# Kernel optimization log

Hardware: AMD Instinct MI355X
Metric: run time of the kernel (lower is better)

Reference implementation:

```python
import jax, jax.numpy as jnp
import numpy as np

B, S, D, H, E = 4, 2048, 512, 8, 4  # batch, seq, embed, heads, expand
HD = D // H


def setup_inputs() -> dict:
    key = jax.random.key(0)
    ks = jax.random.split(key, 9)
    s = lambda k, shape, fan: jax.random.normal(k, shape, jnp.float32) * (fan ** -0.5)
    return {
        "x": jax.random.normal(ks[0], (B, S, D), jnp.float32),
        "Wq": s(ks[1], (D, D), D),
        "Wk": s(ks[2], (D, D), D),
        "Wv": s(ks[3], (D, D), D),
        "Wo": s(ks[4], (D, D), D),
        "W1": s(ks[5], (D, D * E), D),
        "b1": jnp.zeros((D * E,), jnp.float32),
        "W2": s(ks[6], (D * E, D), D * E),
        "b2": jnp.zeros((D,), jnp.float32),
    }


def _encoder_layer(x, Wq, Wk, Wv, Wo, W1, b1, W2, b2):
    # NOTE: source computes InstanceNorm1d twice but discards both results -> no-ops.
    scale = D ** -0.25  # applied to BOTH q and k (net 1/sqrt(embed_dim))
    q = (x @ Wq).reshape(B, S, H, HD).transpose(0, 2, 1, 3) * scale  # [B,H,S,hd]
    k = (x @ Wk).reshape(B, S, H, HD).transpose(0, 2, 1, 3) * scale
    v = (x @ Wv).reshape(B, S, H, HD).transpose(0, 2, 1, 3)
    scores = jnp.einsum('bhqd,bhkd->bhqk', q, k)  # [B,H,S,S]
    attn = jax.nn.softmax(scores, axis=-1)
    o = jnp.einsum('bhqk,bhkd->bhqd', attn, v)  # [B,H,S,hd]
    o = o.transpose(0, 2, 1, 3).reshape(B, S, D)
    x = o @ Wo + x  # residual 1
    h = jax.nn.gelu(x @ W1 + b1, approximate=True)  # torch GELU(approximate='tanh')
    return h @ W2 + b2 + x  # residual 2 (dropout=0, eval)


def reference(x, Wq, Wk, Wv, Wo, W1, b1, W2, b2):
    return _encoder_layer(x, Wq, Wk, Wv, Wo, W1, b1, W2, b2)
```

## Files before the change

kernel.cpp:

```cpp
#include <hip/hip_runtime.h>
#include <hip/hip_bf16.h>


typedef __bf16 bf16;
typedef __attribute__((ext_vector_type(8))) __bf16 bf16x8;
typedef __attribute__((ext_vector_type(4))) __bf16 bf16x4;
typedef __attribute__((ext_vector_type(4))) float f32x4;
typedef __attribute__((ext_vector_type(16))) float f32x16;
typedef __attribute__((ext_vector_type(2))) unsigned int u32x2;
typedef __attribute__((ext_vector_type(4))) unsigned int u32x4;

#define LOG2E 1.4426950408889634f
#define SCORE_SCALE 0.044194173824159216f
#define SCALE_L2E (SCORE_SCALE * LOG2E)
#define FIXED_M 12.0f

#if __has_builtin(__builtin_amdgcn_exp2f)
#define EXP2(x) __builtin_amdgcn_exp2f(x)
#else
#define EXP2(x) exp2f(x)
#endif

__device__ __forceinline__ void gl_lds16(const bf16* g, bf16* l) {
  __builtin_amdgcn_global_load_lds(
      (const __attribute__((address_space(1))) unsigned int*)g,
      (__attribute__((address_space(3))) unsigned int*)l, 16, 0, 0);
}

template <int N>
__device__ __forceinline__ void wait_vm_barrier() {
  if constexpr (N == 0)
    asm volatile("s_waitcnt vmcnt(0)\ns_barrier" ::: "memory");
  else if constexpr (N == 3)
    asm volatile("s_waitcnt vmcnt(3)\ns_barrier" ::: "memory");
  else if constexpr (N == 4)
    asm volatile("s_waitcnt vmcnt(4)\ns_barrier" ::: "memory");
}

__device__ __forceinline__ float gelu_tanh(float x) {
  float u = 0.7978845608028654f * (x + 0.044715f * x * x * x);
  float e = EXP2(u * (2.0f * LOG2E));
  float th = 1.0f - 2.0f / (e + 1.0f);
  return 0.5f * x * (1.0f + th);
}

__device__ __forceinline__ f32x4 mfma_bf16(bf16x8 a, bf16x8 b, f32x4 c) {
  return __builtin_amdgcn_mfma_f32_16x16x32_bf16(a, b, c, 0, 0, 0);
}
__device__ __forceinline__ f32x16 mfma32x16(bf16x8 a, bf16x8 b, f32x16 c) {
  return __builtin_amdgcn_mfma_f32_32x32x16_bf16(a, b, c, 0, 0, 0);
}

__device__ __forceinline__ void plswap(unsigned int& a, unsigned int& b) {
  asm volatile("v_permlane32_swap_b32 %0, %1" : "+v"(a), "+v"(b));
}

template <int MODE, typename OutT, int TN>
__global__ __launch_bounds__(256, 2) void gemm_bt(
    const bf16* __restrict__ A, const bf16* __restrict__ Bt,
    OutT* __restrict__ C, const float* __restrict__ bias,
    const float* __restrict__ resf, const bf16* __restrict__ resb,
    bf16* __restrict__ vt, int M, int N, int K) {
  constexpr int MI = (TN == 128) ? 4 : 2;
  constexpr int NBUF = (TN == 128) ? 2 : 3;
  __shared__ __align__(16) bf16 sA[NBUF][128 * 32];
  __shared__ __align__(16) bf16 sB[NBUF][TN * 32];
  const int tid = threadIdx.x;
  const int lane = tid & 63;
  const int quad = lane >> 4, lc = lane & 15;
  const int wave = tid >> 6;
  const int wr = (TN == 128) ? (wave >> 1) : wave;
  const int wc = (TN == 128) ? (wave & 1) : 0;
  const int m0 = blockIdx.y * 128, n0 = blockIdx.x * TN;

  const int srow = tid >> 2;
  const int kc = (tid & 3) * 8;
  const bf16* Ag1 = A + (size_t)(m0 + srow) * K + kc;
  const bf16* Ag2 = A + (size_t)(m0 + 64 + srow) * K + kc;
  const bf16* Bg1 = Bt + (size_t)(n0 + srow) * K + kc;
  const bf16* Bg2 = Bt + (size_t)(n0 + 64 + srow) * K + kc;
  const int o1 = tid * 8, o2 = (tid + 256) * 8;

  f32x4 acc[MI][4];
#pragma unroll
  for (int mi = 0; mi < MI; ++mi)
#pragma unroll
    for (int ni = 0; ni < 4; ++ni) acc[mi][ni] = (f32x4){0.f, 0.f, 0.f, 0.f};

  const int kIters = K >> 5;

  if constexpr (TN == 128) {
    gl_lds16(Ag1, sA[0] + o1);
    gl_lds16(Ag2, sA[0] + o2);
    gl_lds16(Bg1, sB[0] + o1);
    gl_lds16(Bg2, sB[0] + o2);
    Ag1 += 32; Ag2 += 32; Bg1 += 32; Bg2 += 32;

    for (int kt = 0; kt < kIters; ++kt) {
      __syncthreads();
      const bf16* cA = sA[kt & 1];
      const bf16* cB = sB[kt & 1];
      if (kt + 1 < kIters) {
        bf16* nA = sA[(kt + 1) & 1];
        bf16* nB = sB[(kt + 1) & 1];
        gl_lds16(Ag1, nA + o1);
        gl_lds16(Ag2, nA + o2);
        gl_lds16(Bg1, nB + o1);
        gl_lds16(Bg2, nB + o2);
        Ag1 += 32; Ag2 += 32; Bg1 += 32; Bg2 += 32;
      }
      bf16x8 af[MI], bfm[4];
#pragma unroll
      for (int i = 0; i < MI; ++i)
        af[i] = *(const bf16x8*)(cA +
                                 ((wr * 64 + i * 16 + lc) * 32 + quad * 8));
#pragma unroll
      for (int i = 0; i < 4; ++i)
        bfm[i] =
            *(const bf16x8*)(cB + ((wc * 64 + i * 16 + lc) * 32 + quad * 8));
#pragma unroll
      for (int mi = 0; mi < MI; ++mi)
#pragma unroll
        for (int ni = 0; ni < 4; ++ni)
          acc[mi][ni] = mfma_bf16(af[mi], bfm[ni], acc[mi][ni]);
    }
  } else {
    auto stage = [&](int t) {
      bf16* a = sA[t % 3];
      bf16* bb = sB[t % 3];
      gl_lds16(Ag1 + t * 32, a + o1);
      gl_lds16(Ag2 + t * 32, a + o2);
      gl_lds16(Bg1 + t * 32, bb + o1);
    };
    stage(0);
    stage(1);
    for (int kt = 0; kt < kIters; ++kt) {
      if (kt + 1 < kIters)
        wait_vm_barrier<3>();
      else
        wait_vm_barrier<0>();
      if (kt + 2 < kIters) stage(kt + 2);
      const bf16* cA = sA[kt % 3];
      const bf16* cB = sB[kt % 3];
      bf16x8 af[MI], bfm[4];
#pragma unroll
      for (int i = 0; i < MI; ++i)
        af[i] = *(const bf16x8*)(cA +
                                 ((wr * 32 + i * 16 + lc) * 32 + quad * 8));
#pragma unroll
      for (int i = 0; i < 4; ++i)
        bfm[i] = *(const bf16x8*)(cB + ((i * 16 + lc) * 32 + quad * 8));
#pragma unroll
      for (int mi = 0; mi < MI; ++mi)
#pragma unroll
        for (int ni = 0; ni < 4; ++ni)
          acc[mi][ni] = mfma_bf16(af[mi], bfm[ni], acc[mi][ni]);
    }
  }

  if constexpr (MODE == 0) {
    if (n0 >= 1024) {
#pragma unroll
      for (int mi = 0; mi < MI; ++mi) {
        const int row0 = m0 + wr * (16 * MI) + mi * 16 + quad * 4;
        const int bb = row0 >> 11, s0 = row0 & 2047;
#pragma unroll
        for (int ni = 0; ni < 4; ++ni) {
          const int col = n0 + wc * 64 + ni * 16 + lc;
          const int hh = (col >> 6) & 7, d = col & 63;
          bf16x4 pb;
#pragma unroll
          for (int r = 0; r < 4; ++r) pb[r] = (bf16)acc[mi][ni][r];
          *(bf16x4*)(vt + ((size_t)((bb * 8 + hh) * 64 + d)) * 2048 + s0) = pb;
        }
      }
      return;
    }
  }
#pragma unroll
  for (int mi = 0; mi < MI; ++mi) {
#pragma unroll
    for (int r = 0; r < 4; ++r) {
      const int row = m0 + wr * (16 * MI) + mi * 16 + quad * 4 + r;
#pragma unroll
      for (int ni = 0; ni < 4; ++ni) {
        const int col = n0 + wc * 64 + ni * 16 + lc;
        const size_t idx = (size_t)row * N + col;
        float v = acc[mi][ni][r];
        if (MODE == 1) v += resf[idx];
        if (MODE == 2) v = gelu_tanh(v + bias[col]);
        if (MODE == 3) v += bias[col] + (float)resb[idx];
        C[idx] = (OutT)v;
      }
    }
  }
}

__global__ __launch_bounds__(256, 2) void flash_attn(
    const bf16* __restrict__ QKV, const bf16* __restrict__ Vt,
    bf16* __restrict__ O) {
  const int tid = threadIdx.x;
  const int lane = tid & 63, wave = tid >> 6;
  const int lo5 = lane & 31, hi = lane >> 5;
  const int lin = blockIdx.y * 16 + blockIdx.x;
  const int xcd = lin & 7, slot = lin >> 3;
  const int bh = xcd * 4 + (slot >> 4);
  const int qt = slot & 15;
  const int b = bh >> 3, h = bh & 7;
  const int q0 = qt * 128 + wave * 32;

  __shared__ __align__(16) bf16 sK[3][4096];
  __shared__ __align__(16) bf16 sV[3][4096];

  const bf16* Qrow = QKV + (size_t)(b * 2048 + q0 + lo5) * 1536 + h * 64;
  bf16x8 qf[4];
#pragma unroll
  for (int i = 0; i < 4; ++i) qf[i] = *(const bf16x8*)(Qrow + i * 16 + hi * 8);

  const int colsw = (((lane & 7) ^ (lane >> 3)) << 3);
  const bf16* Kg0 = QKV + (size_t)b * 2048 * 1536 + 512 + (size_t)h * 64 +
                    (size_t)(wave * 16 + (lane >> 3)) * 1536 + colsw;
  const bf16* Vg0 = Vt + (size_t)bh * 64 * 2048 +
                    (size_t)(wave * 16 + (lane >> 3)) * 2048 + colsw;
  const int stag = wave * 1024;
  const int m7 = lo5 & 7;

  f32x16 oacc[2];
  oacc[0] = (f32x16)(0.f);
  oacc[1] = (f32x16)(0.f);
  float rs0 = 0.f, rs1 = 0.f, rs2 = 0.f, rs3 = 0.f;

  auto stage = [&](int t) {
    bf16* dk = sK[t % 3] + stag;
    bf16* dv = sV[t % 3] + stag;
    gl_lds16(Kg0 + (size_t)t * 64 * 1536, dk);
    gl_lds16(Kg0 + (size_t)(t * 64 + 8) * 1536, dk + 512);
    gl_lds16(Vg0 + t * 64, dv);
    gl_lds16(Vg0 + t * 64 + 8 * 2048, dv + 512);
  };
  stage(0);
  stage(1);

  for (int kt = 0; kt < 32; ++kt) {
    if (kt == 31)
      wait_vm_barrier<0>();
    else
      wait_vm_barrier<4>();
    if (kt + 2 < 32) stage(kt + 2);
    const bf16* cK = sK[kt % 3];
    const bf16* cV = sV[kt % 3];

    bf16x8 vf[2][4];
#pragma unroll
    for (int dh = 0; dh < 2; ++dh) {
      const int Rd = dh * 32 + lo5;
#pragma unroll
      for (int w = 0; w < 4; ++w)
        vf[dh][w] =
            *(const bf16x8*)(cV + Rd * 64 + (((2 * w + hi) ^ m7) << 3));
    }

    bf16x8 paw[4];
#pragma unroll
    for (int hl = 0; hl < 2; ++hl) {
      f32x16 st = (f32x16)(0.f);
      const int R = hl * 32 + lo5;
      __builtin_amdgcn_s_setprio(1);
#pragma unroll
      for (int i = 0; i < 4; ++i) {
        bf16x8 kf =
            *(const bf16x8*)(cK + R * 64 + (((2 * i + hi) ^ m7) << 3));
        st = mfma32x16(kf, qf[i], st);
      }
      __builtin_amdgcn_s_setprio(0);
      unsigned int q32[4][2];
#pragma unroll
      for (int g = 0; g < 4; ++g) {
        bf16x4 pb;
        float p0 = EXP2(st[4 * g + 0] * SCALE_L2E - FIXED_M);
        float p1 = EXP2(st[4 * g + 1] * SCALE_L2E - FIXED_M);
        float p2 = EXP2(st[4 * g + 2] * SCALE_L2E - FIXED_M);
        float p3 = EXP2(st[4 * g + 3] * SCALE_L2E - FIXED_M);
        rs0 += p0; rs1 += p1; rs2 += p2; rs3 += p3;
        pb[0] = (bf16)p0; pb[1] = (bf16)p1; pb[2] = (bf16)p2; pb[3] = (bf16)p3;
        u32x2 w2 = __builtin_bit_cast(u32x2, pb);
        q32[g][0] = w2[0];
        q32[g][1] = w2[1];
      }
#pragma unroll
      for (int t = 0; t < 2; ++t) {
        unsigned int a0 = q32[2 * t][0], a1 = q32[2 * t][1];
        unsigned int b0 = q32[2 * t + 1][0], b1 = q32[2 * t + 1][1];
        plswap(a0, b0);
        plswap(a1, b1);
        u32x4 f = {a0, a1, b0, b1};
        paw[hl * 2 + t] = __builtin_bit_cast(bf16x8, f);
      }
    }

    __builtin_amdgcn_s_setprio(1);
#pragma unroll
    for (int dh = 0; dh < 2; ++dh)
#pragma unroll
      for (int w = 0; w < 4; ++w)
        oacc[dh] = mfma32x16(paw[w], vf[dh][w], oacc[dh]);
    __builtin_amdgcn_s_setprio(0);
  }

  float rsum = (rs0 + rs1) + (rs2 + rs3);
  rsum += __shfl_xor(rsum, 32, 64);
  const size_t obase = (size_t)(b * 2048 + q0) * 512 + h * 64;
#pragma unroll
  for (int r = 0; r < 16; ++r) {
    const int qloc = (r & 3) + 8 * (r >> 2) + 4 * hi;
    const float inv = 1.0f / __shfl(rsum, qloc, 64);
#pragma unroll
    for (int dh = 0; dh < 2; ++dh)
      O[obase + (size_t)qloc * 512 + dh * 32 + lo5] =
          (bf16)(oacc[dh][r] * inv);
  }
}

__global__ __launch_bounds__(256) void prep(
    const float* __restrict__ x, const float* __restrict__ Wq,
    const float* __restrict__ Wk, const float* __restrict__ Wv,
    const float* __restrict__ Wo, const float* __restrict__ W1,
    const float* __restrict__ W2, bf16* __restrict__ xb,
    bf16* __restrict__ WqkvT, bf16* __restrict__ WoT, bf16* __restrict__ W1T,
    bf16* __restrict__ W2T) {
  const int bid = blockIdx.x;
  if (bid < 4096) {
    const size_t i = ((size_t)bid * 256 + threadIdx.x) * 4;
    const float4 v = *(const float4*)(x + i);
    bf16x4 o;
    o[0] = (bf16)v.x; o[1] = (bf16)v.y; o[2] = (bf16)v.z; o[3] = (bf16)v.w;
    *(bf16x4*)(xb + i) = o;
    return;
  }
  const int t = bid - 4096;
  const float* in;
  bf16* out;
  int in_ld, out_ld, bx, by;
  if (t < 1024) {
    const int q = t >> 8, r = t & 255;
    bx = r & 15; by = r >> 4; in_ld = 512; out_ld = 512;
    in = (q == 0) ? Wq : (q == 1) ? Wk : (q == 2) ? Wv : Wo;
    out = (q == 0) ? WqkvT
          : (q == 1) ? WqkvT + 512 * 512
          : (q == 2) ? WqkvT + 2 * 512 * 512
                     : WoT;
  } else if (t < 2048) {
    const int r = t - 1024;
    bx = r & 63; by = r >> 6; in_ld = 2048; out_ld = 512;
    in = W1; out = W1T;
  } else {
    const int r = t - 2048;
    bx = r & 15; by = r >> 4; in_ld = 512; out_ld = 2048;
    in = W2; out = W2T;
  }
  __shared__ __align__(16) bf16 tl[32][33];
  const int tx = threadIdx.x & 31, ty = threadIdx.x >> 5;
  const int n0 = bx * 32, k0 = by * 32;
#pragma unroll
  for (int i = 0; i < 4; ++i)
    tl[ty + 8 * i][tx] = (bf16)in[(size_t)(k0 + ty + 8 * i) * in_ld + n0 + tx];
  __syncthreads();
#pragma unroll
  for (int i = 0; i < 4; ++i)
    out[(size_t)(n0 + ty + 8 * i) * out_ld + k0 + tx] = tl[tx][ty + 8 * i];
}

extern "C" void kernel_launch(void* const* d_in, const int* in_sizes, int n_in,
                              void* d_out, int out_size, void* d_ws,
                              size_t ws_size, hipStream_t stream) {
  const float* x = (const float*)d_in[0];
  const float* Wq = (const float*)d_in[1];
  const float* Wk = (const float*)d_in[2];
  const float* Wv = (const float*)d_in[3];
  const float* Wo = (const float*)d_in[4];
  const float* W1 = (const float*)d_in[5];
  const float* b1 = (const float*)d_in[6];
  const float* W2 = (const float*)d_in[7];
  const float* b2 = (const float*)d_in[8];
  float* out = (float*)d_out;

  char* ws = (char*)d_ws;
  size_t off = 0;
  auto alloc = [&](size_t bytes) {
    char* p = ws + off;
    off += (bytes + 255) & ~(size_t)255;
    return p;
  };
  bf16* WqkvT = (bf16*)alloc(1536ULL * 512 * 2);
  bf16* WoT = (bf16*)alloc(512ULL * 512 * 2);
  bf16* W1T = (bf16*)alloc(2048ULL * 512 * 2);
  bf16* W2T = (bf16*)alloc(512ULL * 2048 * 2);
  bf16* xb = (bf16*)alloc(8192ULL * 512 * 2);
  bf16* QKV = (bf16*)alloc(8192ULL * 1536 * 2);
  bf16* Vt = (bf16*)alloc(32ULL * 64 * 2048 * 2);
  bf16* attn = (bf16*)alloc(8192ULL * 512 * 2);
  bf16* x2 = xb;
  bf16* hbuf = QKV;

  const dim3 tb(256);
  prep<<<dim3(7168), tb, 0, stream>>>(x, Wq, Wk, Wv, Wo, W1, W2, xb, WqkvT,
                                      WoT, W1T, W2T);
  gemm_bt<0, bf16, 128><<<dim3(12, 64), tb, 0, stream>>>(
      xb, WqkvT, QKV, nullptr, nullptr, nullptr, Vt, 8192, 1536, 512);
  flash_attn<<<dim3(16, 32), tb, 0, stream>>>(QKV, Vt, attn);
  gemm_bt<1, bf16, 64><<<dim3(8, 64), tb, 0, stream>>>(
      attn, WoT, x2, nullptr, x, nullptr, nullptr, 8192, 512, 512);
  gemm_bt<2, bf16, 128><<<dim3(16, 64), tb, 0, stream>>>(
      x2, W1T, hbuf, b1, nullptr, nullptr, nullptr, 8192, 2048, 512);
  gemm_bt<3, float, 64><<<dim3(8, 64), tb, 0, stream>>>(
      hbuf, W2T, out, b2, nullptr, x2, nullptr, 8192, 512, 2048);
}
```

Baseline: 247.0 us.

## Load K/V tiles directly into registers instead of staging through LDS

Replaces the triple-buffered LDS staging of K and V tiles with direct global-to-register loads, double-buffered in two register sets (A/B). This removes LDS traffic and the barriers between iterations. It also interleaves the softmax of the second half-tile with the PV MFMAs of the first half. In exchange, each wave fetches K/V separately from global memory or L2 with no sharing across the block's waves, which raises global traffic about fourfold. It also increases register pressure, which may hurt occupancy under launch_bounds(256,2).

Result: slower. 328.0 us (+32.8%).

```diff
diff --git a/kernel.cpp b/kernel.cpp
--- a/kernel.cpp
+++ b/kernel.cpp
@@ -209,102 +209,97 @@
   const int b = bh >> 3, h = bh & 7;
   const int q0 = qt * 128 + wave * 32;
 
-  __shared__ __align__(16) bf16 sK[3][4096];
-  __shared__ __align__(16) bf16 sV[3][4096];
-
   const bf16* Qrow = QKV + (size_t)(b * 2048 + q0 + lo5) * 1536 + h * 64;
   bf16x8 qf[4];
 #pragma unroll
   for (int i = 0; i < 4; ++i) qf[i] = *(const bf16x8*)(Qrow + i * 16 + hi * 8);
 
-  const int colsw = (((lane & 7) ^ (lane >> 3)) << 3);
-  const bf16* Kg0 = QKV + (size_t)b * 2048 * 1536 + 512 + (size_t)h * 64 +
-                    (size_t)(wave * 16 + (lane >> 3)) * 1536 + colsw;
-  const bf16* Vg0 = Vt + (size_t)bh * 64 * 2048 +
-                    (size_t)(wave * 16 + (lane >> 3)) * 2048 + colsw;
-  const int stag = wave * 1024;
-  const int m7 = lo5 & 7;
+  const bf16* Kl = QKV + (size_t)b * 2048 * 1536 + 512 + (size_t)h * 64 +
+                   (size_t)lo5 * 1536 + hi * 8;
+  const bf16* Vl = Vt + (size_t)bh * 64 * 2048 + (size_t)lo5 * 2048 + hi * 8;
 
   f32x16 oacc[2];
   oacc[0] = (f32x16)(0.f);
   oacc[1] = (f32x16)(0.f);
   float rs0 = 0.f, rs1 = 0.f, rs2 = 0.f, rs3 = 0.f;
 
-  auto stage = [&](int t) {
-    bf16* dk = sK[t % 3] + stag;
-    bf16* dv = sV[t % 3] + stag;
-    gl_lds16(Kg0 + (size_t)t * 64 * 1536, dk);
-    gl_lds16(Kg0 + (size_t)(t * 64 + 8) * 1536, dk + 512);
-    gl_lds16(Vg0 + t * 64, dv);
-    gl_lds16(Vg0 + t * 64 + 8 * 2048, dv + 512);
-  };
-  stage(0);
-  stage(1);
-
-  for (int kt = 0; kt < 32; ++kt) {
-    if (kt == 31)
-      wait_vm_barrier<0>();
-    else
-      wait_vm_barrier<4>();
-    if (kt + 2 < 32) stage(kt + 2);
-    const bf16* cK = sK[kt % 3];
-    const bf16* cV = sV[kt % 3];
-
-    bf16x8 vf[2][4];
-#pragma unroll
-    for (int dh = 0; dh < 2; ++dh) {
-      const int Rd = dh * 32 + lo5;
+  bf16x8 kfA[2][4], vfA[2][4], kfB[2][4], vfB[2][4];
+
+  auto loadT = [&](bf16x8(&kf)[2][4], bf16x8(&vf)[2][4], int t) {
+#pragma unroll
+    for (int hl = 0; hl < 2; ++hl)
+#pragma unroll
+      for (int i = 0; i < 4; ++i)
+        kf[hl][i] = *(const bf16x8*)(Kl + ((size_t)(t * 64 + hl * 32)) * 1536 +
+                                     i * 16);
+#pragma unroll
+    for (int dh = 0; dh < 2; ++dh)
 #pragma unroll
       for (int w = 0; w < 4; ++w)
         vf[dh][w] =
-            *(const bf16x8*)(cV + Rd * 64 + (((2 * w + hi) ^ m7) << 3));
-    }
-
-    bf16x8 paw[4];
-#pragma unroll
-    for (int hl = 0; hl < 2; ++hl) {
-      f32x16 st = (f32x16)(0.f);
-      const int R = hl * 32 + lo5;
-      __builtin_amdgcn_s_setprio(1);
-#pragma unroll
-      for (int i = 0; i < 4; ++i) {
-        bf16x8 kf =
-            *(const bf16x8*)(cK + R * 64 + (((2 * i + hi) ^ m7) << 3));
-        st = mfma32x16(kf, qf[i], st);
-      }
-      __builtin_amdgcn_s_setprio(0);
-      unsigned int q32[4][2];
-#pragma unroll
-      for (int g = 0; g < 4; ++g) {
-        bf16x4 pb;
-        float p0 = EXP2(st[4 * g + 0] * SCALE_L2E - FIXED_M);
-        float p1 = EXP2(st[4 * g + 1] * SCALE_L2E - FIXED_M);
-        float p2 = EXP2(st[4 * g + 2] * SCALE_L2E - FIXED_M);
-        float p3 = EXP2(st[4 * g + 3] * SCALE_L2E - FIXED_M);
-        rs0 += p0; rs1 += p1; rs2 += p2; rs3 += p3;
-        pb[0] = (bf16)p0; pb[1] = (bf16)p1; pb[2] = (bf16)p2; pb[3] = (bf16)p3;
-        u32x2 w2 = __builtin_bit_cast(u32x2, pb);
-        q32[g][0] = w2[0];
-        q32[g][1] = w2[1];
-      }
-#pragma unroll
-      for (int t = 0; t < 2; ++t) {
-        unsigned int a0 = q32[2 * t][0], a1 = q32[2 * t][1];
-        unsigned int b0 = q32[2 * t + 1][0], b1 = q32[2 * t + 1][1];
-        plswap(a0, b0);
-        plswap(a1, b1);
-        u32x4 f = {a0, a1, b0, b1};
-        paw[hl * 2 + t] = __builtin_bit_cast(bf16x8, f);
-      }
-    }
-
+            *(const bf16x8*)(Vl + (size_t)dh * 32 * 2048 + t * 64 + w * 16);
+  };
+
+  bf16x8 paw[4];
+
+  auto softmax = [&](const f32x16& st, int hl) {
+    unsigned int q32[4][2];
+#pragma unroll
+    for (int g = 0; g < 4; ++g) {
+      bf16x4 pb;
+      float p0 = EXP2(st[4 * g + 0] * SCALE_L2E - FIXED_M);
+      float p1 = EXP2(st[4 * g + 1] * SCALE_L2E - FIXED_M);
+      float p2 = EXP2(st[4 * g + 2] * SCALE_L2E - FIXED_M);
+      float p3 = EXP2(st[4 * g + 3] * SCALE_L2E - FIXED_M);
+      rs0 += p0; rs1 += p1; rs2 += p2; rs3 += p3;
+      pb[0] = (bf16)p0; pb[1] = (bf16)p1; pb[2] = (bf16)p2; pb[3] = (bf16)p3;
+      u32x2 w2 = __builtin_bit_cast(u32x2, pb);
+      q32[g][0] = w2[0];
+      q32[g][1] = w2[1];
+    }
+#pragma unroll
+    for (int t = 0; t < 2; ++t) {
+      unsigned int a0 = q32[2 * t][0], a1 = q32[2 * t][1];
+      unsigned int b0 = q32[2 * t + 1][0], b1 = q32[2 * t + 1][1];
+      plswap(a0, b0);
+      plswap(a1, b1);
+      u32x4 f = {a0, a1, b0, b1};
+      paw[hl * 2 + t] = __builtin_bit_cast(bf16x8, f);
+    }
+  };
+
+  auto computeT = [&](const bf16x8(&kf)[2][4], const bf16x8(&vf)[2][4]) {
+    f32x16 st0 = (f32x16)(0.f), st1 = (f32x16)(0.f);
     __builtin_amdgcn_s_setprio(1);
 #pragma unroll
-    for (int dh = 0; dh < 2; ++dh)
-#pragma unroll
-      for (int w = 0; w < 4; ++w)
-        oacc[dh] = mfma32x16(paw[w], vf[dh][w], oacc[dh]);
+    for (int i = 0; i < 4; ++i) {
+      st0 = mfma32x16(kf[0][i], qf[i], st0);
+      st1 = mfma32x16(kf[1][i], qf[i], st1);
+    }
     __builtin_amdgcn_s_setprio(0);
+    softmax(st0, 0);
+#pragma unroll
+    for (int w = 0; w < 2; ++w) {
+      oacc[0] = mfma32x16(paw[w], vf[0][w], oacc[0]);
+      oacc[1] = mfma32x16(paw[w], vf[1][w], oacc[1]);
+    }
+    softmax(st1, 1);
+    __builtin_amdgcn_s_setprio(1);
+#pragma unroll
+    for (int w = 2; w < 4; ++w) {
+      oacc[0] = mfma32x16(paw[w], vf[0][w], oacc[0]);
+      oacc[1] = mfma32x16(paw[w], vf[1][w], oacc[1]);
+    }
+    __builtin_amdgcn_s_setprio(0);
+  };
+
+  loadT(kfA, vfA, 0);
+  loadT(kfB, vfB, 1);
+  for (int t = 0; t < 32; t += 2) {
+    computeT(kfA, vfA);
+    if (t + 2 < 32) loadT(kfA, vfA, t + 2);
+    computeT(kfB, vfB);
+    if (t + 3 < 32) loadT(kfB, vfB, t + 3);
   }
 
   float rsum = (rs0 + rs1) + (rs2 + rs3);
```
